# Optimization experiments

Hardware: AMD Instinct MI355X
Metric: run time of the kernel (lower is better)

## Reference

```python
import jax, jax.numpy as jnp
import numpy as np

T, B, D, H, R, S, M = 1024, 16, 512, 8, 32, 16, 16
TQ = R + T + S   # query length
KL = M + R + T   # key/value length
NEG_INF = -1e8


def setup_inputs() -> dict:
    key = jax.random.key(0)
    ks = jax.random.split(key, 12)
    utterance = jax.random.normal(ks[0], (T, B, D), jnp.float32)
    right_context = jax.random.normal(ks[1], (R, B, D), jnp.float32)
    summary = jax.random.normal(ks[2], (S, B, D), jnp.float32)
    mems = jax.random.normal(ks[3], (M, B, D), jnp.float32)
    # valid lengths in [T//2, T]; force max == T so data-dependent shapes are static
    lengths = jax.random.randint(ks[4], (B,), T // 2, T + 1).at[0].set(T).astype(jnp.int64)
    # block-streaming style mask: query i may only attend to keys <= i + M
    q_idx = jnp.arange(TQ)[:, None]
    k_idx = jnp.arange(KL)[None, :]
    attention_mask = k_idx > (q_idx + M)  # True = masked
    scale = 0.02
    Wq = jax.random.normal(ks[5], (D, D), jnp.float32) * scale
    bq = jnp.zeros((D,), jnp.float32)
    Wkv = jax.random.normal(ks[6], (2 * D, D), jnp.float32) * scale
    bkv = jnp.zeros((2 * D,), jnp.float32)
    Wo = jax.random.normal(ks[7], (D, D), jnp.float32) * scale
    bo = jnp.zeros((D,), jnp.float32)
    return dict(utterance=utterance, lengths=lengths, right_context=right_context,
                summary=summary, mems=mems, attention_mask=attention_mask,
                Wq=Wq, bq=bq, Wkv=Wkv, bkv=bkv, Wo=Wo, bo=bo)


def _split_heads(x):
    # (L, B, D) -> (B*H, L, D//H), matching torch .view(-1, B*H, d).transpose(0, 1)
    L = x.shape[0]
    return x.reshape(L, B * H, D // H).transpose(1, 0, 2)


def reference(utterance, lengths, right_context, summary, mems, attention_mask,
              Wq, bq, Wkv, bkv, Wo, bo):
    d_head = D // H
    scaling = d_head ** -0.5

    query_in = jnp.concatenate([right_context, utterance, summary], axis=0)   # (TQ, B, D)
    kv_in = jnp.concatenate([mems, right_context, utterance], axis=0)         # (KL, B, D)

    query = query_in @ Wq.T + bq
    kv = kv_in @ Wkv.T + bkv
    k, v = jnp.split(kv, 2, axis=2)

    q = _split_heads(query)  # (B*H, TQ, d)
    kh = _split_heads(k)     # (B*H, KL, d)
    vh = _split_heads(v)

    w = jnp.einsum('nqd,nkd->nqk', q * scaling, kh).astype(jnp.float32)
    w = jnp.where(attention_mask[None, :, :], NEG_INF, w)

    # padding mask (B > 1 path): klengths = lengths + M + right_context_blocks_length
    rcbl = TQ - jnp.max(lengths) - S  # == R since max(lengths) == T
    klengths = lengths + M + rcbl
    pad_mask = jnp.arange(KL)[None, :] >= klengths[:, None]  # (B, KL)
    w = w.reshape(B, H, TQ, KL)
    w = jnp.where(pad_mask[:, None, None, :], NEG_INF, w)
    w = w.reshape(B * H, TQ, KL)

    probs = jax.nn.softmax(w, axis=-1)  # dropout p=0.0
    attn = jnp.einsum('nqk,nkd->nqd', probs, vh)          # (B*H, TQ, d)
    attn = attn.transpose(1, 0, 2).reshape(TQ, B, D)

    out = attn @ Wo.T + bo                                # (TQ, B, D)
    output_right_context = out[:TQ - S]                    # (R+T, B, D)
    output_mems = jnp.clip(out[TQ - S:], -10.0, 10.0)      # tanh_on_mem=False
    return output_right_context, output_mems[:-1]          # (S-1, B, D)
```

## Files before the change

### kernel.cpp

```cpp
#include <hip/hip_runtime.h>

#define T_   1024
#define B_   16
#define D_   512
#define H_   8
#define R_   32
#define S_   16
#define M_   16
#define TQ_  1072
#define KL_  1072
#define DH_  64
#define NROW 17152
#define K_   512
#define LQ_  268
#define QSCALE 0.18033688f

typedef unsigned short u16;
using bf16x8 = __attribute__((ext_vector_type(8))) short;
using f32x4  = __attribute__((ext_vector_type(4))) float;
using u16x4  = __attribute__((ext_vector_type(4))) unsigned short;

__device__ __forceinline__ u16 f2bf(float f) {
    unsigned int u = __builtin_bit_cast(unsigned int, f);
    unsigned int r = u + 0x7fffu + ((u >> 16) & 1u);
    return (u16)(r >> 16);
}

__device__ __forceinline__ unsigned int cvt_pk_bf16(float a, float b) {
    unsigned int r;
    asm("v_cvt_pk_bf16_f32 %0, %1, %2" : "=v"(r) : "v"(a), "v"(b));
    return r;
}

__device__ __forceinline__ void gload_lds16(const u16* g, u16* l) {
    __builtin_amdgcn_global_load_lds(
        (const __attribute__((address_space(1))) unsigned int*)g,
        (__attribute__((address_space(3))) unsigned int*)l,
        16, 0, 0);
}

__device__ __forceinline__ int xcd_swz(int bid, int nwg) {
    const int q = nwg >> 3, r = nwg & 7;
    const int xcd = bid & 7, idx = bid >> 3;
    return (xcd < r ? xcd * (q + 1) : r * (q + 1) + (xcd - r) * q) + idx;
}

__global__ void k_convert4(const float4* __restrict__ utt, const float4* __restrict__ rc,
                           const float4* __restrict__ smr, const float4* __restrict__ mems,
                           const float4* __restrict__ Wq, const float4* __restrict__ Wkv,
                           const float4* __restrict__ Wo,
                           u16x4* __restrict__ xall,
                           u16x4* __restrict__ wq, u16x4* __restrict__ wkv,
                           u16x4* __restrict__ wo)
{
    const int N4 = 17408 * D_ / 4;
    const int MB = M_ * B_ * D_ / 4;
    const int RB = MB + R_ * B_ * D_ / 4;
    const int UB = RB + T_ * B_ * D_ / 4;
    const int W1 = D_ * D_ / 4, W2 = 2 * D_ * D_ / 4;
    for (int i = blockIdx.x * blockDim.x + threadIdx.x; i < N4;
         i += gridDim.x * blockDim.x) {
        float4 v;
        if (i < MB)      v = mems[i];
        else if (i < RB) v = rc[i - MB];
        else if (i < UB) v = utt[i - RB];
        else             v = smr[i - UB];
        xall[i] = (u16x4){f2bf(v.x), f2bf(v.y), f2bf(v.z), f2bf(v.w)};
        if (i < W1) { v = Wq[i];  wq[i]  = (u16x4){f2bf(v.x), f2bf(v.y), f2bf(v.z), f2bf(v.w)}; }
        if (i < W2) { v = Wkv[i]; wkv[i] = (u16x4){f2bf(v.x), f2bf(v.y), f2bf(v.z), f2bf(v.w)}; }
        if (i < W1) { v = Wo[i];  wo[i]  = (u16x4){f2bf(v.x), f2bf(v.y), f2bf(v.z), f2bf(v.w)}; }
    }
}

template<bool TOR>
__device__ __forceinline__ void pipe_core(const u16* __restrict__ Ab,
                                          const u16* __restrict__ Wb,
                                          u16* lds, f32x4* acc)
{
    u16* As0 = lds;
    u16* As1 = lds + 256 * 64;
    u16* Bs0 = lds + 2 * 256 * 64;
    u16* Bs1 = lds + 2 * 256 * 64 + 128 * 64;

    const int tid  = threadIdx.x;
    const int wid  = tid >> 6, lane = tid & 63;
    const int wm   = wid >> 1, wn = wid & 1;
    const int col  = lane & 15, quad = lane >> 4;
    const int sr   = tid >> 3;
    const int sc   = (tid & 7) ^ (sr & 7);
    const u16* gA  = Ab + (size_t)sr * K_ + sc * 8;
    const u16* gB  = Wb + (size_t)sr * K_ + sc * 8;

#pragma unroll
    for (int i = 0; i < 16; i++) acc[i] = (f32x4){0.f, 0.f, 0.f, 0.f};

    auto stage = [&](int kt, u16* Au, u16* Bu) {
#pragma unroll
        for (int i = 0; i < 4; i++)
            gload_lds16(gA + (size_t)(i * 64) * K_ + kt * 64,
                        Au + (i * 64 + wid * 8) * 64);
#pragma unroll
        for (int j = 0; j < 2; j++)
            gload_lds16(gB + (size_t)(j * 64) * K_ + kt * 64,
                        Bu + (j * 64 + wid * 8) * 64);
    };

    stage(0, As0, Bs0);

    u16 *Ac = As0, *Bc = Bs0, *An = As1, *Bn = Bs1;
    for (int kt = 0; kt < 8; ++kt) {
        __builtin_amdgcn_s_barrier();
        if (kt < 7) {
            stage(kt + 1, An, Bn);
            asm volatile("s_waitcnt vmcnt(6)" ::: "memory");
        } else {
            asm volatile("s_waitcnt vmcnt(0)" ::: "memory");
        }
        __builtin_amdgcn_s_barrier();
        __builtin_amdgcn_sched_barrier(0);
#pragma unroll
        for (int kh = 0; kh < 2; ++kh) {
            bf16x8 aF[4], bF[4];
#pragma unroll
            for (int mi = 0; mi < 4; mi++)
                aF[mi] = *(const bf16x8*)&Ac[(wm * 64 + mi * 16 + col) * 64
                             + (((kh * 4 + quad) ^ (col & 7)) * 8)];
#pragma unroll
            for (int ni = 0; ni < 4; ni++)
                bF[ni] = *(const bf16x8*)&Bc[(wn * 64 + ni * 16 + col) * 64
                             + (((kh * 4 + quad) ^ (col & 7)) * 8)];
            __builtin_amdgcn_s_setprio(1);
            if (TOR) {
#pragma unroll
                for (int ni = 0; ni < 4; ni++)
#pragma unroll
                    for (int mi = 0; mi < 4; mi++)
                        acc[ni * 4 + mi] = __builtin_amdgcn_mfma_f32_16x16x32_bf16(
                            bF[ni], aF[mi], acc[ni * 4 + mi], 0, 0, 0);
            } else {
#pragma unroll
                for (int mi = 0; mi < 4; mi++)
#pragma unroll
                    for (int ni = 0; ni < 4; ni++)
                        acc[mi * 4 + ni] = __builtin_amdgcn_mfma_f32_16x16x32_bf16(
                            aF[mi], bF[ni], acc[mi * 4 + ni], 0, 0, 0);
            }
            __builtin_amdgcn_s_setprio(0);
        }
        u16* t;
        t = Ac; Ac = An; An = t;
        t = Bc; Bc = Bn; Bn = t;
    }
}

__global__ __launch_bounds__(512, 2)
void k_gemm_qkv8(const u16* __restrict__ xall,
                 const u16* __restrict__ wqp, const u16* __restrict__ wkvp,
                 const float* __restrict__ bq, const float* __restrict__ bkv,
                 u16* __restrict__ qb, u16* __restrict__ kb, u16* __restrict__ vt)
{
    extern __shared__ u16 lds[];
    const int wgid = xcd_swz(blockIdx.x, 67 * 12);
    const int tn = wgid % 12, tm = wgid / 12;
    const int typ = tn >> 2, sub = tn & 3;
    const u16* Ab = (typ == 0 ? xall + (size_t)256 * K_ : xall)
                    + (size_t)tm * 256 * K_;
    const u16* Wb = (typ == 0 ? wqp : wkvp + (typ == 2 ? (size_t)512 * K_ : 0))
                    + (size_t)sub * 128 * K_;

    const int wid = threadIdx.x >> 6, lane = threadIdx.x & 63;
    const int wm = wid >> 1, wn = wid & 1;
    const int col = lane & 15, quad = lane >> 4;

    f32x4 acc[16];
    if (typ == 2) {
        pipe_core<false>(Ab, Wb, lds, acc);
#pragma unroll
        for (int ni = 0; ni < 4; ni++) {
            const int f = sub * 128 + wn * 64 + ni * 16 + col;
            const float bs = bkv[512 + f];
            const int lq = tm * 4 + wm;
#pragma unroll
            for (int r = 0; r < 4; r++) {
                const int bb = quad * 4 + r;
                uint2 pk;
                pk.x = cvt_pk_bf16(acc[0 * 4 + ni][r] + bs,
                                   acc[1 * 4 + ni][r] + bs);
                pk.y = cvt_pk_bf16(acc[2 * 4 + ni][r] + bs,
                                   acc[3 * 4 + ni][r] + bs);
                *(uint2*)&vt[(((size_t)bb * LQ_ + lq) * 512 + f) * 4] = pk;
            }
        }
    } else {
        pipe_core<true>(Ab, Wb, lds, acc);
        const float* bias = (typ == 0) ? bq : bkv;
        u16* outp = (typ == 0) ? qb : kb;
        const float qs = (typ == 0) ? QSCALE : 1.0f;
#pragma unroll
        for (int ni = 0; ni < 4; ni++) {
            const int gc0 = sub * 128 + wn * 64 + ni * 16 + quad * 4;
            const float4 bs4 = *(const float4*)&bias[gc0];
#pragma unroll
            for (int mi = 0; mi < 4; mi++) {
                const int mrow = tm * 256 + wm * 64 + mi * 16 + col;
                f32x4 a = acc[ni * 4 + mi];
                uint2 pk;
                pk.x = cvt_pk_bf16((a[0] + bs4.x) * qs, (a[1] + bs4.y) * qs);
                pk.y = cvt_pk_bf16((a[2] + bs4.z) * qs, (a[3] + bs4.w) * qs);
                *(uint2*)&outp[(size_t)mrow * 512 + gc0] = pk;
            }
        }
    }
}

__global__ __launch_bounds__(512, 2)
void k_gemm_o8(const u16* __restrict__ A, const u16* __restrict__ W,
               const float* __restrict__ bias, float* __restrict__ Co)
{
    extern __shared__ u16 lds[];
    const int wgid = xcd_swz(blockIdx.x, 67 * 4);
    const int tn = wgid % 4, tm = wgid / 4;
    const u16* Ab = A + (size_t)tm * 256 * K_;
    const u16* Wb = W + (size_t)tn * 128 * K_;

    const int wid = threadIdx.x >> 6, lane = threadIdx.x & 63;
    const int wm = wid >> 1, wn = wid & 1;
    const int col = lane & 15, quad = lane >> 4;

    f32x4 acc[16];
    pipe_core<true>(Ab, Wb, lds, acc);

#pragma unroll
    for (int ni = 0; ni < 4; ni++) {
        const int gc0 = tn * 128 + wn * 64 + ni * 16 + quad * 4;
        const float4 bs4 = *(const float4*)&bias[gc0];
#pragma unroll
        for (int mi = 0; mi < 4; mi++) {
            const int l = tm * 16 + wm * 4 + mi;
            if (l == TQ_ - 1) continue;
            const int mrow = tm * 256 + wm * 64 + mi * 16 + col;
            f32x4 a = acc[ni * 4 + mi];
            float4 v = {a[0] + bs4.x, a[1] + bs4.y, a[2] + bs4.z, a[3] + bs4.w};
            if (l >= TQ_ - S_) {
                v.x = fminf(10.0f, fmaxf(-10.0f, v.x));
                v.y = fminf(10.0f, fmaxf(-10.0f, v.y));
                v.z = fminf(10.0f, fmaxf(-10.0f, v.z));
                v.w = fminf(10.0f, fmaxf(-10.0f, v.w));
            }
            *(float4*)&Co[(size_t)mrow * 512 + gc0] = v;
        }
    }
}

__global__ __launch_bounds__(256, 2)
void k_attn5(const u16* __restrict__ qbuf, const u16* __restrict__ kb,
             const u16* __restrict__ vt, const int* __restrict__ lenp,
             u16* __restrict__ attnb)
{
    __shared__ __align__(16) u16 Ks[2][64 * 64];
    __shared__ __align__(16) u16 Vs[2][64 * 64];
    __shared__ __align__(16) u16 Ps[4][16 * 64];

    const int blk  = blockIdx.x;
    const int qblk = 16 - (blk >> 7);
    const int bh   = blk & 127;
    const int b = bh >> 3, h = bh & 7;
    const int tid = threadIdx.x;
    const int w = tid >> 6, lane = tid & 63;
    const int col = lane & 15, quad = lane >> 4;

    int stride = (lenp[1] == 0) ? 2 : 1;
    int maxlen = 0;
    for (int i = 0; i < B_; i++) maxlen = max(maxlen, lenp[i * stride]);
    const int klen = lenp[b * stride] + M_ + (TQ_ - maxlen - S_);

    const int q0 = qblk * 64;
    const int qw = q0 + w * 16;
    const int q  = qw + col;

    int qrow = min(q, TQ_ - 1);
    const u16* qp = qbuf + ((size_t)qrow * B_ + b) * D_ + h * DH_ + quad * 8;
    bf16x8 bq0 = *(const bf16x8*)(qp);
    bf16x8 bq1 = *(const bf16x8*)(qp + 32);

    const int s0 = tid, s1 = tid + 256;
    const u16* kbase = kb + (size_t)b * 512 + h * DH_;
    size_t kof0 = (size_t)(s0 >> 3) * 8192 + (size_t)(((s0 & 7) ^ ((s0 >> 3) & 7)) * 8);
    size_t kof1 = (size_t)(s1 >> 3) * 8192 + (size_t)(((s1 & 7) ^ ((s1 >> 3) & 7)) * 8);
    const u16* vbase = vt + ((size_t)b * LQ_ * 512 + (size_t)h * DH_) * 4;
    auto vchunk = [](int s) -> size_t {
        int fp = s >> 4;
        int lq = (s & 15) ^ (fp & 15);
        return (size_t)lq * 2048 + (size_t)fp * 8;
    };
    const size_t vof0 = vchunk(s0), vof1 = vchunk(s1);

    float li = 0.f;
    f32x4 o[4];
#pragma unroll
    for (int g = 0; g < 4; g++) o[g] = (f32x4){0.f, 0.f, 0.f, 0.f};

    const int nk = min(q0 + 64 + M_, klen);
    const int numkt = (nk + 63) >> 6;
    u16* pw = &Ps[w][0];

    gload_lds16(kbase + kof0, &Ks[0][(size_t)w * 512]);
    gload_lds16(kbase + kof1, &Ks[0][2048 + (size_t)w * 512]);
    gload_lds16(vbase + vof0, &Vs[0][(size_t)w * 512]);
    gload_lds16(vbase + vof1, &Vs[0][2048 + (size_t)w * 512]);

    for (int kt = 0; kt < numkt; kt++) {
        const int kn0 = kt * 64;
        const int cur = kt & 1;
        __syncthreads();
        if (kt + 1 < numkt) {
            const size_t kstep = (size_t)(kn0 + 64) * 8192;
            const size_t vstep = (size_t)(kt + 1) * 32768;
            gload_lds16(kbase + kstep + kof0, &Ks[cur ^ 1][(size_t)w * 512]);
            gload_lds16(kbase + kstep + kof1, &Ks[cur ^ 1][2048 + (size_t)w * 512]);
            gload_lds16(vbase + vstep + vof0, &Vs[cur ^ 1][(size_t)w * 512]);
            gload_lds16(vbase + vstep + vof1, &Vs[cur ^ 1][2048 + (size_t)w * 512]);
        }

        f32x4 sc[4];
        __builtin_amdgcn_s_setprio(1);
#pragma unroll
        for (int g = 0; g < 4; g++) {
            int key = g * 16 + col;
            bf16x8 a0 = *(const bf16x8*)&Ks[cur][key * 64 + ((quad ^ (key & 7)) * 8)];
            bf16x8 a1 = *(const bf16x8*)&Ks[cur][key * 64 + (((4 + quad) ^ (key & 7)) * 8)];
            f32x4 z = {0.f, 0.f, 0.f, 0.f};
            z = __builtin_amdgcn_mfma_f32_16x16x32_bf16(a0, bq0, z, 0, 0, 0);
            z = __builtin_amdgcn_mfma_f32_16x16x32_bf16(a1, bq1, z, 0, 0, 0);
            sc[g] = z;
        }
        __builtin_amdgcn_s_setprio(0);

        const bool needmask = (kn0 + 63 > qw + M_) || (kn0 + 63 >= klen);
        if (needmask) {
#pragma unroll
            for (int g = 0; g < 4; g++)
#pragma unroll
                for (int r = 0; r < 4; r++) {
                    int key = kn0 + g * 16 + quad * 4 + r;
                    bool valid = (key <= q + M_) && (key < klen);
                    sc[g][r] = valid ? sc[g][r] : -1e8f;
                }
        }

#pragma unroll
        for (int g = 0; g < 4; g++) {
            float pr[4];
#pragma unroll
            for (int r = 0; r < 4; r++) {
                pr[r] = __builtin_amdgcn_exp2f(sc[g][r]);
                li += pr[r];
            }
            uint2 pk;
            pk.x = cvt_pk_bf16(pr[0], pr[1]);
            pk.y = cvt_pk_bf16(pr[2], pr[3]);
            int kc = g * 2 + (quad >> 1);
            *(uint2*)&pw[col * 64 + ((kc ^ (col & 7)) * 8) + (quad & 1) * 4] = pk;
        }

        bf16x8 ap0 = *(const bf16x8*)&pw[col * 64 + ((quad ^ (col & 7)) * 8)];
        bf16x8 ap1 = *(const bf16x8*)&pw[col * 64 + (((4 + quad) ^ (col & 7)) * 8)];
        __builtin_amdgcn_s_setprio(1);
#pragma unroll
        for (int g = 0; g < 4; g++) {
            int d = g * 16 + col;
            int fp = d >> 1, fo = (d & 1) * 4;
            bf16x8 bv[2];
#pragma unroll
            for (int hh = 0; hh < 2; hh++) {
                int lqA = hh * 8 + quad * 2;
                int posA = fp * 16 + (lqA ^ (fp & 15));
                int posB = fp * 16 + ((lqA + 1) ^ (fp & 15));
                u16x4 loA = *(const u16x4*)&Vs[cur][posA * 8 + fo];
                u16x4 loB = *(const u16x4*)&Vs[cur][posB * 8 + fo];
                bf16x8 t;
                t[0] = loA[0]; t[1] = loA[1]; t[2] = loA[2]; t[3] = loA[3];
                t[4] = loB[0]; t[5] = loB[1]; t[6] = loB[2]; t[7] = loB[3];
                bv[hh] = t;
            }
            o[g] = __builtin_amdgcn_mfma_f32_16x16x32_bf16(bv[0], ap0, o[g], 0, 0, 0);
            o[g] = __builtin_amdgcn_mfma_f32_16x16x32_bf16(bv[1], ap1, o[g], 0, 0, 0);
        }
        __builtin_amdgcn_s_setprio(0);
    }

    li += __shfl_xor(li, 16);
    li += __shfl_xor(li, 32);
    const float inv = 1.0f / li;
    const int qo = qw + col;
    if (qw + 16 <= TQ_) {
#pragma unroll
        for (int g = 0; g < 4; g++) {
            uint2 pk;
            pk.x = cvt_pk_bf16(o[g][0] * inv, o[g][1] * inv);
            pk.y = cvt_pk_bf16(o[g][2] * inv, o[g][3] * inv);
            *(uint2*)&attnb[((size_t)qo * B_ + b) * D_ + h * DH_ + g * 16 + quad * 4] = pk;
        }
    }
}

extern "C" void kernel_launch(void* const* d_in, const int* in_sizes, int n_in,
                              void* d_out, int out_size, void* d_ws, size_t ws_size,
                              hipStream_t stream)
{
    const float* utt  = (const float*)d_in[0];
    const int*   len  = (const int*)  d_in[1];
    const float* rc   = (const float*)d_in[2];
    const float* smr  = (const float*)d_in[3];
    const float* mems = (const float*)d_in[4];
    const float* Wq   = (const float*)d_in[6];
    const float* bq   = (const float*)d_in[7];
    const float* Wkv  = (const float*)d_in[8];
    const float* bkv  = (const float*)d_in[9];
    const float* Wo   = (const float*)d_in[10];
    const float* bo   = (const float*)d_in[11];

    char* ws = (char*)d_ws;
    size_t off = 0;
    auto alloc = [&](size_t bytes) -> void* {
        void* p = ws + off;
        off += (bytes + 255) & ~(size_t)255;
        return p;
    };
    u16* xall = (u16*)alloc((size_t)17408 * D_ * 2);
    u16* wq   = (u16*)alloc((size_t)D_ * D_ * 2);
    u16* wkv  = (u16*)alloc((size_t)2 * D_ * D_ * 2);
    u16* wo   = (u16*)alloc((size_t)D_ * D_ * 2);
    u16* qb   = (u16*)alloc((size_t)NROW * D_ * 2);
    u16* kb   = (u16*)alloc((size_t)NROW * D_ * 2);
    u16* vt   = (u16*)alloc((size_t)B_ * LQ_ * 512 * 4 * 2 + 65536);
    u16* attnb = xall;

    static int s_attr_done = 0;
    if (!s_attr_done) {
        hipFuncSetAttribute(reinterpret_cast<const void*>(k_gemm_qkv8),
                            hipFuncAttributeMaxDynamicSharedMemorySize, 98304);
        hipFuncSetAttribute(reinterpret_cast<const void*>(k_gemm_o8),
                            hipFuncAttributeMaxDynamicSharedMemorySize, 98304);
        s_attr_done = 1;
    }

    k_convert4<<<2048, 256, 0, stream>>>((const float4*)utt, (const float4*)rc,
                                         (const float4*)smr, (const float4*)mems,
                                         (const float4*)Wq, (const float4*)Wkv,
                                         (const float4*)Wo,
                                         (u16x4*)xall,
                                         (u16x4*)wq, (u16x4*)wkv, (u16x4*)wo);
    k_gemm_qkv8<<<67 * 12, 512, 98304, stream>>>(xall, wq, wkv, bq, bkv, qb, kb, vt);
    k_attn5<<<17 * 128, 256, 0, stream>>>(qb, kb, vt, len, attnb);
    k_gemm_o8<<<67 * 4, 512, 98304, stream>>>(attnb, wo, bo, (float*)d_out);
}
```

Measured before the change: 217.2 us.

## Shrink GEMM tiles to 128x128 single-buffered with 256-thread blocks

Replaces the 256x128 double-buffered async-load GEMM core with a 128x128 tile using static LDS, a single buffer and plain __syncthreads, launched with 256 threads and a 4-blocks-per-CU bound. The grid doubles along M, and the V-transpose epilogue is adjusted to write half-width packed pairs. The aim is more resident blocks per CU and better wave balance across CUs, giving occupancy-based latency hiding in place of explicit prefetch. The cost is lost load/compute overlap inside a block, the dropped setprio hint, and a smaller tile that reloads B more often.

```diff
diff --git a/kernel.cpp b/kernel.cpp
--- a/kernel.cpp
+++ b/kernel.cpp
@@ -73,18 +73,15 @@
 }
 
 template<bool TOR>
-__device__ __forceinline__ void pipe_core(const u16* __restrict__ Ab,
-                                          const u16* __restrict__ Wb,
-                                          u16* lds, f32x4* acc)
-{
-    u16* As0 = lds;
-    u16* As1 = lds + 256 * 64;
-    u16* Bs0 = lds + 2 * 256 * 64;
-    u16* Bs1 = lds + 2 * 256 * 64 + 128 * 64;
+__device__ __forceinline__ void core128(const u16* __restrict__ Ab,
+                                        const u16* __restrict__ Wb,
+                                        f32x4* acc)
+{
+    __shared__ __align__(16) u16 As[128 * 64];
+    __shared__ __align__(16) u16 Bs[128 * 64];
 
     const int tid  = threadIdx.x;
-    const int wid  = tid >> 6, lane = tid & 63;
-    const int wm   = wid >> 1, wn = wid & 1;
+    const int w    = tid >> 6, lane = tid & 63;
     const int col  = lane & 15, quad = lane >> 4;
     const int sr   = tid >> 3;
     const int sc   = (tid & 7) ^ (sr & 7);
@@ -94,116 +91,95 @@
 #pragma unroll
     for (int i = 0; i < 16; i++) acc[i] = (f32x4){0.f, 0.f, 0.f, 0.f};
 
-    auto stage = [&](int kt, u16* Au, u16* Bu) {
+    for (int kt = 0; kt < 8; ++kt) {
+        __syncthreads();
 #pragma unroll
         for (int i = 0; i < 4; i++)
-            gload_lds16(gA + (size_t)(i * 64) * K_ + kt * 64,
-                        Au + (i * 64 + wid * 8) * 64);
-#pragma unroll
-        for (int j = 0; j < 2; j++)
-            gload_lds16(gB + (size_t)(j * 64) * K_ + kt * 64,
-                        Bu + (j * 64 + wid * 8) * 64);
-    };
-
-    stage(0, As0, Bs0);
-
-    u16 *Ac = As0, *Bc = Bs0, *An = As1, *Bn = Bs1;
-    for (int kt = 0; kt < 8; ++kt) {
-        __builtin_amdgcn_s_barrier();
-        if (kt < 7) {
-            stage(kt + 1, An, Bn);
-            asm volatile("s_waitcnt vmcnt(6)" ::: "memory");
-        } else {
-            asm volatile("s_waitcnt vmcnt(0)" ::: "memory");
-        }
-        __builtin_amdgcn_s_barrier();
-        __builtin_amdgcn_sched_barrier(0);
+            gload_lds16(gA + (size_t)(i * 32) * K_ + kt * 64,
+                        &As[(i * 32 + w * 8) * 64]);
+#pragma unroll
+        for (int i = 0; i < 4; i++)
+            gload_lds16(gB + (size_t)(i * 32) * K_ + kt * 64,
+                        &Bs[(i * 32 + w * 8) * 64]);
+        __syncthreads();
 #pragma unroll
         for (int kh = 0; kh < 2; ++kh) {
-            bf16x8 aF[4], bF[4];
-#pragma unroll
-            for (int mi = 0; mi < 4; mi++)
-                aF[mi] = *(const bf16x8*)&Ac[(wm * 64 + mi * 16 + col) * 64
+            bf16x8 aF[2], bF[8];
+#pragma unroll
+            for (int mi = 0; mi < 2; mi++)
+                aF[mi] = *(const bf16x8*)&As[(w * 32 + mi * 16 + col) * 64
                              + (((kh * 4 + quad) ^ (col & 7)) * 8)];
 #pragma unroll
-            for (int ni = 0; ni < 4; ni++)
-                bF[ni] = *(const bf16x8*)&Bc[(wn * 64 + ni * 16 + col) * 64
+            for (int ni = 0; ni < 8; ni++)
+                bF[ni] = *(const bf16x8*)&Bs[(ni * 16 + col) * 64
                              + (((kh * 4 + quad) ^ (col & 7)) * 8)];
-            __builtin_amdgcn_s_setprio(1);
             if (TOR) {
 #pragma unroll
-                for (int ni = 0; ni < 4; ni++)
-#pragma unroll
-                    for (int mi = 0; mi < 4; mi++)
-                        acc[ni * 4 + mi] = __builtin_amdgcn_mfma_f32_16x16x32_bf16(
-                            bF[ni], aF[mi], acc[ni * 4 + mi], 0, 0, 0);
+                for (int ni = 0; ni < 8; ni++)
+#pragma unroll
+                    for (int mi = 0; mi < 2; mi++)
+                        acc[ni * 2 + mi] = __builtin_amdgcn_mfma_f32_16x16x32_bf16(
+                            bF[ni], aF[mi], acc[ni * 2 + mi], 0, 0, 0);
             } else {
 #pragma unroll
-                for (int mi = 0; mi < 4; mi++)
-#pragma unroll
-                    for (int ni = 0; ni < 4; ni++)
-                        acc[mi * 4 + ni] = __builtin_amdgcn_mfma_f32_16x16x32_bf16(
-                            aF[mi], bF[ni], acc[mi * 4 + ni], 0, 0, 0);
-            }
-            __builtin_amdgcn_s_setprio(0);
-        }
-        u16* t;
-        t = Ac; Ac = An; An = t;
-        t = Bc; Bc = Bn; Bn = t;
-    }
-}
-
-__global__ __launch_bounds__(512, 2)
-void k_gemm_qkv8(const u16* __restrict__ xall,
+                for (int mi = 0; mi < 2; mi++)
+#pragma unroll
+                    for (int ni = 0; ni < 8; ni++)
+                        acc[mi * 8 + ni] = __builtin_amdgcn_mfma_f32_16x16x32_bf16(
+                            aF[mi], bF[ni], acc[mi * 8 + ni], 0, 0, 0);
+            }
+        }
+    }
+}
+
+__global__ __launch_bounds__(256, 4)
+void k_gemm_qkv9(const u16* __restrict__ xall,
                  const u16* __restrict__ wqp, const u16* __restrict__ wkvp,
                  const float* __restrict__ bq, const float* __restrict__ bkv,
                  u16* __restrict__ qb, u16* __restrict__ kb, u16* __restrict__ vt)
 {
-    extern __shared__ u16 lds[];
-    const int wgid = xcd_swz(blockIdx.x, 67 * 12);
+    const int wgid = xcd_swz(blockIdx.x, 134 * 12);
     const int tn = wgid % 12, tm = wgid / 12;
     const int typ = tn >> 2, sub = tn & 3;
     const u16* Ab = (typ == 0 ? xall + (size_t)256 * K_ : xall)
-                    + (size_t)tm * 256 * K_;
+                    + (size_t)tm * 128 * K_;
     const u16* Wb = (typ == 0 ? wqp : wkvp + (typ == 2 ? (size_t)512 * K_ : 0))
                     + (size_t)sub * 128 * K_;
 
-    const int wid = threadIdx.x >> 6, lane = threadIdx.x & 63;
-    const int wm = wid >> 1, wn = wid & 1;
+    const int tid = threadIdx.x;
+    const int w = tid >> 6, lane = tid & 63;
     const int col = lane & 15, quad = lane >> 4;
 
     f32x4 acc[16];
     if (typ == 2) {
-        pipe_core<false>(Ab, Wb, lds, acc);
-#pragma unroll
-        for (int ni = 0; ni < 4; ni++) {
-            const int f = sub * 128 + wn * 64 + ni * 16 + col;
+        core128<false>(Ab, Wb, acc);
+        const int lq = tm * 2 + (w >> 1);
+        const int so = (w & 1) * 2;
+#pragma unroll
+        for (int ni = 0; ni < 8; ni++) {
+            const int f = sub * 128 + ni * 16 + col;
             const float bs = bkv[512 + f];
-            const int lq = tm * 4 + wm;
 #pragma unroll
             for (int r = 0; r < 4; r++) {
                 const int bb = quad * 4 + r;
-                uint2 pk;
-                pk.x = cvt_pk_bf16(acc[0 * 4 + ni][r] + bs,
-                                   acc[1 * 4 + ni][r] + bs);
-                pk.y = cvt_pk_bf16(acc[2 * 4 + ni][r] + bs,
-                                   acc[3 * 4 + ni][r] + bs);
-                *(uint2*)&vt[(((size_t)bb * LQ_ + lq) * 512 + f) * 4] = pk;
+                unsigned int pk = cvt_pk_bf16(acc[0 * 8 + ni][r] + bs,
+                                              acc[1 * 8 + ni][r] + bs);
+                *(unsigned int*)&vt[(((size_t)bb * LQ_ + lq) * 512 + f) * 4 + so] = pk;
             }
         }
     } else {
-        pipe_core<true>(Ab, Wb, lds, acc);
+        core128<true>(Ab, Wb, acc);
         const float* bias = (typ == 0) ? bq : bkv;
         u16* outp = (typ == 0) ? qb : kb;
         const float qs = (typ == 0) ? QSCALE : 1.0f;
 #pragma unroll
-        for (int ni = 0; ni < 4; ni++) {
-            const int gc0 = sub * 128 + wn * 64 + ni * 16 + quad * 4;
+        for (int ni = 0; ni < 8; ni++) {
+            const int gc0 = sub * 128 + ni * 16 + quad * 4;
             const float4 bs4 = *(const float4*)&bias[gc0];
 #pragma unroll
-            for (int mi = 0; mi < 4; mi++) {
-                const int mrow = tm * 256 + wm * 64 + mi * 16 + col;
-                f32x4 a = acc[ni * 4 + mi];
+            for (int mi = 0; mi < 2; mi++) {
+                const int mrow = tm * 128 + w * 32 + mi * 16 + col;
+                f32x4 a = acc[ni * 2 + mi];
                 uint2 pk;
                 pk.x = cvt_pk_bf16((a[0] + bs4.x) * qs, (a[1] + bs4.y) * qs);
                 pk.y = cvt_pk_bf16((a[2] + bs4.z) * qs, (a[3] + bs4.w) * qs);
@@ -213,33 +189,32 @@
     }
 }
 
-__global__ __launch_bounds__(512, 2)
-void k_gemm_o8(const u16* __restrict__ A, const u16* __restrict__ W,
+__global__ __launch_bounds__(256, 4)
+void k_gemm_o9(const u16* __restrict__ A, const u16* __restrict__ W,
                const float* __restrict__ bias, float* __restrict__ Co)
 {
-    extern __shared__ u16 lds[];
-    const int wgid = xcd_swz(blockIdx.x, 67 * 4);
+    const int wgid = xcd_swz(blockIdx.x, 134 * 4);
     const int tn = wgid % 4, tm = wgid / 4;
-    const u16* Ab = A + (size_t)tm * 256 * K_;
+    const u16* Ab = A + (size_t)tm * 128 * K_;
     const u16* Wb = W + (size_t)tn * 128 * K_;
 
-    const int wid = threadIdx.x >> 6, lane = threadIdx.x & 63;
-    const int wm = wid >> 1, wn = wid & 1;
+    const int tid = threadIdx.x;
+    const int w = tid >> 6, lane = tid & 63;
     const int col = lane & 15, quad = lane >> 4;
 
     f32x4 acc[16];
-    pipe_core<true>(Ab, Wb, lds, acc);
-
-#pragma unroll
-    for (int ni = 0; ni < 4; ni++) {
-        const int gc0 = tn * 128 + wn * 64 + ni * 16 + quad * 4;
+    core128<true>(Ab, Wb, acc);
+
+#pragma unroll
+    for (int ni = 0; ni < 8; ni++) {
+        const int gc0 = tn * 128 + ni * 16 + quad * 4;
         const float4 bs4 = *(const float4*)&bias[gc0];
 #pragma unroll
-        for (int mi = 0; mi < 4; mi++) {
-            const int l = tm * 16 + wm * 4 + mi;
+        for (int mi = 0; mi < 2; mi++) {
+            const int l = tm * 8 + w * 2 + mi;
             if (l == TQ_ - 1) continue;
-            const int mrow = tm * 256 + wm * 64 + mi * 16 + col;
-            f32x4 a = acc[ni * 4 + mi];
+            const int mrow = tm * 128 + w * 32 + mi * 16 + col;
+            f32x4 a = acc[ni * 2 + mi];
             float4 v = {a[0] + bs4.x, a[1] + bs4.y, a[2] + bs4.z, a[3] + bs4.w};
             if (l >= TQ_ - S_) {
                 v.x = fminf(10.0f, fmaxf(-10.0f, v.x));
@@ -436,22 +411,13 @@
     u16* vt   = (u16*)alloc((size_t)B_ * LQ_ * 512 * 4 * 2 + 65536);
     u16* attnb = xall;
 
-    static int s_attr_done = 0;
-    if (!s_attr_done) {
-        hipFuncSetAttribute(reinterpret_cast<const void*>(k_gemm_qkv8),
-                            hipFuncAttributeMaxDynamicSharedMemorySize, 98304);
-        hipFuncSetAttribute(reinterpret_cast<const void*>(k_gemm_o8),
-                            hipFuncAttributeMaxDynamicSharedMemorySize, 98304);
-        s_attr_done = 1;
-    }
-
     k_convert4<<<2048, 256, 0, stream>>>((const float4*)utt, (const float4*)rc,
                                          (const float4*)smr, (const float4*)mems,
                                          (const float4*)Wq, (const float4*)Wkv,
                                          (const float4*)Wo,
                                          (u16x4*)xall,
                                          (u16x4*)wq, (u16x4*)wkv, (u16x4*)wo);
-    k_gemm_qkv8<<<67 * 12, 512, 98304, stream>>>(xall, wq, wkv, bq, bkv, qb, kb, vt);
+    k_gemm_qkv9<<<134 * 12, 256, 0, stream>>>(xall, wq, wkv, bq, bkv, qb, kb, vt);
     k_attn5<<<17 * 128, 256, 0, stream>>>(qb, kb, vt, len, attnb);
-    k_gemm_o8<<<67 * 4, 512, 98304, stream>>>(attnb, wo, bo, (float*)d_out);
-}
+    k_gemm_o9<<<134 * 4, 256, 0, stream>>>(attnb, wo, bo, (float*)d_out);
+}
```

New measurement: 215.9 us. Within noise of the previous version (-0.6%).
